# Kernel tuning notes

Hardware: AMD Instinct MI355X
Metric: run time of the kernel (lower is better)

The kernel has to match this reference:

```python
import jax, jax.numpy as jnp
import numpy as np
import math

N = 400000          # nodes at finest depth
E = 2000000         # edges = N * avg_degree
B = 8               # batch of octrees
C_IN = 4            # input feature channels (channel_in)
N_EDGE_TYPE = 5
N_NODE_TYPE = 7     # depth - 1
AVG_DEGREE = 5
C_OUT = 32          # channels[depth_out]
TEMB_CH = 512       # channels[depth_stop]


def swish(v):
    return v * jax.nn.sigmoid(v)


def setup_inputs() -> dict:
    key = jax.random.key(0)
    ks = jax.random.split(key, 12)
    x = jax.random.normal(ks[0], (N, C_IN), jnp.float32)
    t = jax.random.uniform(ks[1], (B,), jnp.float32) * 1000.0
    edge_index = jax.random.randint(ks[2], (2, E), 0, N)
    edge_type = jax.random.randint(ks[3], (E,), 0, N_EDGE_TYPE)
    node_type = jax.random.randint(ks[4], (N,), 0, N_NODE_TYPE)
    batch_id = jax.random.randint(ks[5], (N,), 0, B)
    fan = N_EDGE_TYPE * (C_IN + N_NODE_TYPE)  # 55
    W_conv = jax.random.normal(ks[6], (fan, C_OUT), jnp.float32) / np.sqrt(fan)
    W1 = jax.random.normal(ks[7], (TEMB_CH // 4, TEMB_CH), jnp.float32) / np.sqrt(TEMB_CH // 4)
    b1 = jnp.zeros((TEMB_CH,), jnp.float32)
    W2 = jax.random.normal(ks[8], (TEMB_CH, TEMB_CH), jnp.float32) / np.sqrt(TEMB_CH)
    b2 = jnp.zeros((TEMB_CH,), jnp.float32)
    W_temb = jax.random.normal(ks[9], (TEMB_CH, C_OUT), jnp.float32) / np.sqrt(TEMB_CH)
    return dict(x=x, t=t, edge_index=edge_index, edge_type=edge_type,
                node_type=node_type, batch_id=batch_id, W_conv=W_conv,
                W1=W1, b1=b1, W2=W2, b2=b2, W_temb=W_temb)


def time_embedding(t, W1, b1, W2, b2):
    # TimeEmbedding.forward: sinusoidal embedding -> lin1 -> swish -> lin2
    half = TEMB_CH // 8  # n_channels // 8
    freqs = jnp.exp(jnp.arange(half, dtype=jnp.float32) * (-math.log(10000.0) / (half - 1)))
    ang = t[:, None] * freqs[None, :]             # [B, half]
    emb = jnp.concatenate([jnp.sin(ang), jnp.cos(ang)], axis=1)  # [B, 2*half]
    emb = swish(emb @ W1 + b1)
    return emb @ W2 + b2                           # [B, TEMB_CH]


def graph_conv(x, edge_index, edge_type, node_type, W_conv):
    # dual-octree GraphConv: one-hot node type, per-(node, edge_type) gather-scatter, dense mix
    oh = jax.nn.one_hot(node_type, N_NODE_TYPE, dtype=x.dtype)
    xh = jnp.concatenate([x, oh], axis=1)          # [N, C_IN + N_NODE_TYPE]
    row, col = edge_index[0], edge_index[1]
    idx = row * N_EDGE_TYPE + edge_type            # bucket per (dst node, edge type)
    agg = jax.ops.segment_sum(xh[col], idx, num_segments=N * N_EDGE_TYPE)
    agg = agg.reshape(N, N_EDGE_TYPE * xh.shape[1])
    return (agg @ W_conv) / AVG_DEGREE             # [N, C_OUT]


def reference(x, t, edge_index, edge_type, node_type, batch_id, W_conv, W1, b1, W2, b2, W_temb):
    h = graph_conv(x, edge_index, edge_type, node_type, W_conv)   # conv1 on input features
    temb = time_embedding(t, W1, b1, W2, b2)                       # [B, TEMB_CH]
    inj = swish(temb) @ W_temb                                     # project temb to node channels
    return h + inj[batch_id]                                       # per-node temb injection
```

## Files before the change

kernel.cpp:

```cpp
#include <hip/hip_runtime.h>
#include <hip/hip_fp16.h>


#define CH      4096
#define CW      2048
#define CWSH    11
#define WSZ     128
#define WSH     7
#define NBCMAX  512
#define CAP     2048

__device__ __forceinline__ unsigned pack2(float a, float b) {
    __half2 h = __floats2half2_rn(a, b);
    union { __half2 h; unsigned u; } cv; cv.h = h; return cv.u;
}
__device__ __forceinline__ float2 unpack2(unsigned u) {
    union { unsigned u; __half2 h; } cv; cv.u = u;
    return __half22float2(cv.h);
}

__global__ __launch_bounds__(256) void histW_kernel(
    const int* __restrict__ ei, int* __restrict__ counts,
    const float* __restrict__ x, uint2* __restrict__ xh,
    const float* __restrict__ t, const float* __restrict__ W1,
    float* __restrict__ h1acc, float* __restrict__ h2acc,
    float* __restrict__ inj,
    int E, int N, int NBC, int NCHP)
{
    int tid = threadIdx.x;
    if ((int)blockIdx.x >= NCHP) {
        int b = blockIdx.x - NCHP;
        __shared__ float emb[128];
        if (tid < 128) {
            const float kStep = 9.210340371976184f / 63.0f;
            int k = tid & 63;
            float ang = t[b] * expf(-(float)k * kStep);
            emb[tid] = (tid < 64) ? sinf(ang) : cosf(ang);
        }
        __syncthreads();
        for (int j = tid; j < 512; j += 256) {
            float a = 0.f;
            for (int k = 0; k < 128; ++k) a += emb[k] * W1[k * 512 + j];
            h1acc[b * 512 + j] = a;
            h2acc[b * 512 + j] = 0.f;
        }
        if (tid < 32) inj[b * 32 + tid] = 0.f;
        return;
    }
    __shared__ int h[NBCMAX];
    int c = blockIdx.x;
    for (int i = tid; i < NBC; i += 256) h[i] = 0;
    __syncthreads();
    int s = c * CH, e = min(s + CH, E);
    int nfull = (e - s) & ~3;
    for (int i0 = s + tid * 4; i0 < s + nfull; i0 += 1024) {
        int4 r4 = *(const int4*)&ei[i0];
        atomicAdd(&h[r4.x >> CWSH], 1);
        atomicAdd(&h[r4.y >> CWSH], 1);
        atomicAdd(&h[r4.z >> CWSH], 1);
        atomicAdd(&h[r4.w >> CWSH], 1);
    }
    for (int i = s + nfull + tid; i < e; i += 256)
        atomicAdd(&h[ei[i] >> CWSH], 1);
    __syncthreads();
    int* row = counts + (size_t)c * NBC;
    for (int b = tid; b < NBC; b += 256) row[b] = h[b];
    int per = (N + NCHP - 1) / NCHP;
    int n0 = c * per, n1 = min(n0 + per, N);
    for (int n = n0 + tid; n < n1; n += 256) {
        float4 v = ((const float4*)x)[n];
        uint2 p;
        p.x = pack2(v.x, v.y);
        p.y = pack2(v.z, v.w);
        xh[n] = p;
    }
}

__global__ __launch_bounds__(256) void scanA_kernel(
    const int* __restrict__ counts, int* __restrict__ bsums,
    const float* __restrict__ h1acc, const float* __restrict__ b1,
    const float* __restrict__ W2, float* __restrict__ h2acc,
    int M, int NBC, int LOGC, int nblkA)
{
    int tid = threadIdx.x;
    if ((int)blockIdx.x >= nblkA) {
        int p = blockIdx.x - nblkA;
        __shared__ float h1s[64];
        if (tid < 64) {
            int bb = tid >> 3, kk = tid & 7;
            int k = p * 8 + kk;
            float v = h1acc[bb * 512 + k] + b1[k];
            h1s[tid] = v / (1.f + expf(-v));
        }
        __syncthreads();
        for (int jj = 0; jj < 2; ++jj) {
            int j = tid + jj * 256;
            float acc[8] = {};
#pragma unroll
            for (int kk = 0; kk < 8; ++kk) {
                float w = W2[(p * 8 + kk) * 512 + j];
#pragma unroll
                for (int bb = 0; bb < 8; ++bb) acc[bb] += h1s[bb * 8 + kk] * w;
            }
#pragma unroll
            for (int bb = 0; bb < 8; ++bb)
                atomicAdd(&h2acc[bb * 512 + j], acc[bb]);
        }
        return;
    }
    __shared__ int s[256];
    int j0 = blockIdx.x * 4096 + tid * 16;
    int maskC = (1 << LOGC) - 1;
    int p = 0;
#pragma unroll
    for (int k = 0; k < 16; ++k) {
        int j = j0 + k;
        if (j < M) {
            int b = j >> LOGC, c = j & maskC;
            p += counts[(size_t)c * NBC + b];
        }
    }
    s[tid] = p; __syncthreads();
    for (int off = 128; off > 0; off >>= 1) {
        if (tid < off) s[tid] += s[tid + off];
        __syncthreads();
    }
    if (tid == 0) bsums[blockIdx.x] = s[0];
}

__global__ __launch_bounds__(1024) void scanB_kernel(
    int* __restrict__ bsums, int* __restrict__ bstart, int nblk, int NBC, int E)
{
    __shared__ int s[1024];
    int tid = threadIdx.x;
    int v = (tid < nblk) ? bsums[tid] : 0;
    s[tid] = v; __syncthreads();
    for (int off = 1; off < 1024; off <<= 1) {
        int u = (tid >= off) ? s[tid - off] : 0;
        __syncthreads();
        s[tid] += u;
        __syncthreads();
    }
    if (tid < nblk) bsums[tid] = s[tid] - v;
    if (tid == 0) bstart[NBC] = E;
}

__global__ __launch_bounds__(256) void scanC_kernel(
    const int* __restrict__ counts, const int* __restrict__ bsums,
    int* __restrict__ base, int* __restrict__ bstart,
    const float* __restrict__ h2acc, const float* __restrict__ b2,
    const float* __restrict__ Wt, float* __restrict__ inj,
    int M, int NBC, int LOGC, int nblkA)
{
    int tid = threadIdx.x;
    if ((int)blockIdx.x >= nblkA) {
        int ks = blockIdx.x - nblkA;
        __shared__ float sws[8][64];
        for (int i = tid; i < 512; i += 256) {
            int b = i >> 6, kk = i & 63;
            int k = ks * 64 + kk;
            float v = h2acc[b * 512 + k] + b2[k];
            sws[b][kk] = v / (1.f + expf(-v));
        }
        __syncthreads();
        int b = tid >> 5, c = tid & 31;
        float acc = 0.f;
        for (int kk = 0; kk < 64; ++kk)
            acc += sws[b][kk] * Wt[(ks * 64 + kk) * 32 + c];
        atomicAdd(&inj[tid], acc);
        return;
    }
    __shared__ int s[256];
    int j0 = blockIdx.x * 4096 + tid * 16;
    int maskC = (1 << LOGC) - 1;
    int v[16]; int p = 0;
#pragma unroll
    for (int k = 0; k < 16; ++k) {
        int j = j0 + k;
        v[k] = 0;
        if (j < M) {
            int b = j >> LOGC, c = j & maskC;
            v[k] = counts[(size_t)c * NBC + b];
        }
        p += v[k];
    }
    s[tid] = p; __syncthreads();
    for (int off = 1; off < 256; off <<= 1) {
        int u = (tid >= off) ? s[tid - off] : 0;
        __syncthreads();
        s[tid] += u;
        __syncthreads();
    }
    int run = bsums[blockIdx.x] + (s[tid] - p);
#pragma unroll
    for (int k = 0; k < 16; ++k) {
        int j = j0 + k;
        if (j < M) {
            base[j] = run;
            if ((j & maskC) == 0) bstart[j >> LOGC] = run;
            run += v[k];
        }
    }
}

__global__ __launch_bounds__(512) void scatter_kernel(
    const int* __restrict__ ei, const int* __restrict__ etype,
    const int* __restrict__ ntype, const int* __restrict__ base,
    uint2* __restrict__ rec, int E, int NBC, int LOGC)
{
    __shared__ int cur[NBCMAX];
    int tid = threadIdx.x;
    int nwg = gridDim.x;
    int q = nwg >> 3, r = nwg & 7;
    int xcd = blockIdx.x & 7, idx = blockIdx.x >> 3;
    int c = (xcd < r) ? xcd * (q + 1) + idx
                      : r * (q + 1) + (xcd - r) * q + idx;
    for (int b = tid; b < NBC; b += 512)
        cur[b] = base[((size_t)b << LOGC) + c];
    __syncthreads();
    int s = c * CH, e = min(s + CH, E);
    int nfull = (e - s) & ~3;
    for (int i0 = s + tid * 4; i0 < s + nfull; i0 += 2048) {
        int4 r4 = *(const int4*)&ei[i0];
        int4 c4 = *(const int4*)&ei[E + i0];
        int4 t4 = *(const int4*)&etype[i0];
#pragma unroll
        for (int k = 0; k < 4; ++k) {
            int row = (&r4.x)[k], col = (&c4.x)[k], T = (&t4.x)[k];
            int nt = ntype[col];
            int b = row >> CWSH;
            int slot = atomicAdd(&cur[b], 1);
            uint2 rc;
            rc.x = (unsigned)col | ((unsigned)T << 19) | ((unsigned)nt << 22);
            rc.y = (unsigned)(row & (CW - 1));
            rec[slot] = rc;
        }
    }
    for (int i = s + nfull + tid; i < e; i += 512) {
        int row = ei[i], col = ei[E + i];
        int T = etype[i], nt = ntype[col];
        int b = row >> CWSH;
        int slot = atomicAdd(&cur[b], 1);
        uint2 rc;
        rc.x = (unsigned)col | ((unsigned)T << 19) | ((unsigned)nt << 22);
        rc.y = (unsigned)(row & (CW - 1));
        rec[slot] = rc;
    }
}

__global__ __launch_bounds__(1024) void repack_kernel(
    const int* __restrict__ bstart, const uint2* __restrict__ rec,
    unsigned* __restrict__ rec2, int* __restrict__ nodeStart,
    int NBC, int N, int E)
{
    __shared__ int hist[CW];
    __shared__ int sc[1024];
    int tid = threadIdx.x;
    int b = blockIdx.x;
    for (int i = tid; i < CW; i += 1024) hist[i] = 0;
    __syncthreads();
    int s = bstart[b], e = bstart[b + 1];
    for (int i = s + tid; i < e; i += 1024)
        atomicAdd(&hist[rec[i].y], 1);
    __syncthreads();
    int a0 = hist[2 * tid], a1 = hist[2 * tid + 1];
    int tsum = a0 + a1;
    sc[tid] = tsum; __syncthreads();
    for (int off = 1; off < 1024; off <<= 1) {
        int u = (tid >= off) ? sc[tid - off] : 0;
        __syncthreads();
        sc[tid] += u;
        __syncthreads();
    }
    int excl = sc[tid] - tsum;
    hist[2 * tid]     = s + excl;
    hist[2 * tid + 1] = s + excl + a0;
    __syncthreads();
    int nbase = b * CW;
    for (int l = tid; l < CW; l += 1024) {
        int n = nbase + l;
        if (n < N) nodeStart[n] = hist[l];
    }
    if (b == NBC - 1 && tid == 0) nodeStart[N] = E;
    __syncthreads();
    for (int i = s + tid; i < e; i += 1024) {
        uint2 rc = rec[i];
        int slot = atomicAdd(&hist[rc.y], 1);
        rec2[slot] = rc.x;
    }
}

__global__ __launch_bounds__(512) void consume_kernel(
    const int* __restrict__ nodeStart, const unsigned* __restrict__ rec2,
    const uint2* __restrict__ xh, const float* __restrict__ Wc,
    const int* __restrict__ batch, const float* __restrict__ inj,
    float* __restrict__ out, int N)
{
    __shared__ int seg[WSZ + 1];
    __shared__ unsigned smeta[CAP];
    __shared__ unsigned sx01[CAP];
    __shared__ unsigned sx23[CAP];
    int tid = threadIdx.x;
    int f = blockIdx.x;
    int node0 = f << WSH;
    int nodes = N - node0; if (nodes > WSZ) nodes = WSZ;

    for (int i = tid; i <= nodes; i += 512) seg[i] = nodeStart[node0 + i];
    __syncthreads();
    int s = seg[0], e = seg[nodes];

    int nl = tid & (WSZ - 1);
    int myS = (nl < nodes) ? seg[nl] : e;
    int myE = (nl < nodes) ? seg[nl + 1] : e;

    float acc[20] = {};
    int cnt0[5] = {}, cnt1[5] = {};
    for (int base = s; base < e; base += CAP) {
        int w = e - base; if (w > CAP) w = CAP;
        __syncthreads();
        for (int i = tid; i < w; i += 512) {
            unsigned u = rec2[base + i];
            smeta[i] = u;
            uint2 p = xh[u & 0x7FFFFu];
            sx01[i] = p.x;
            sx23[i] = p.y;
        }
        __syncthreads();
        int lo = myS > base ? myS : base;
        int hi = myE < base + w ? myE : base + w;
        for (int j = lo; j < hi; ++j) {
            int k = j - base;
            unsigned u = smeta[k];
            int T  = (int)((u >> 19) & 7u);
            int nt = (int)((u >> 22) & 7u);
            float2 x01 = unpack2(sx01[k]);
            float2 x23 = unpack2(sx23[k]);
            int lob = (nt < 4) ? (1 << (nt * 8)) : 0;
            int hib = (nt >= 4) ? (1 << ((nt - 4) * 8)) : 0;
#pragma unroll
            for (int tt = 0; tt < 5; ++tt) {
                bool m = (T == tt);
                acc[tt * 4 + 0] += m ? x01.x : 0.f;
                acc[tt * 4 + 1] += m ? x01.y : 0.f;
                acc[tt * 4 + 2] += m ? x23.x : 0.f;
                acc[tt * 4 + 3] += m ? x23.y : 0.f;
                cnt0[tt] += m ? lob : 0;
                cnt1[tt] += m ? hib : 0;
            }
        }
    }

    if (nl < nodes) {
        int hf = __builtin_amdgcn_readfirstlane((int)tid >> 7);
        const float4* wq = (const float4*)Wc;
        float4 o0 = {0.f, 0.f, 0.f, 0.f}, o1 = o0;
#pragma unroll
        for (int f2 = 0; f2 < 55; ++f2) {
            const int tt = f2 / 11, j = f2 % 11;
            float a;
            if (j < 4) a = acc[tt * 4 + j];
            else {
                const int kk = j - 4;
                a = (kk < 4) ? (float)((cnt0[tt] >> (kk * 8)) & 255)
                             : (float)((cnt1[tt] >> ((kk - 4) * 8)) & 255);
            }
            float4 w0 = wq[f2 * 8 + hf * 2];
            float4 w1 = wq[f2 * 8 + hf * 2 + 1];
            o0.x += a * w0.x; o0.y += a * w0.y; o0.z += a * w0.z; o0.w += a * w0.w;
            o1.x += a * w1.x; o1.y += a * w1.y; o1.z += a * w1.z; o1.w += a * w1.w;
        }
        int n = node0 + nl;
        int bb = batch[n];
        const float4* iv = ((const float4*)inj) + bb * 8 + hf * 2;
        float4 i0 = iv[0], i1 = iv[1];
        float4 r0, r1;
        r0.x = i0.x + 0.2f * o0.x; r0.y = i0.y + 0.2f * o0.y;
        r0.z = i0.z + 0.2f * o0.z; r0.w = i0.w + 0.2f * o0.w;
        r1.x = i1.x + 0.2f * o1.x; r1.y = i1.y + 0.2f * o1.y;
        r1.z = i1.z + 0.2f * o1.z; r1.w = i1.w + 0.2f * o1.w;
        float4* op = ((float4*)out) + (size_t)n * 8 + hf * 2;
        op[0] = r0; op[1] = r1;
    }
}

__global__ __launch_bounds__(256) void temb_fused_kernel(
    const float* __restrict__ t,
    const float* __restrict__ W1, const float* __restrict__ b1,
    const float* __restrict__ W2, const float* __restrict__ b2,
    const float* __restrict__ Wt, float* __restrict__ inj)
{
    int b = blockIdx.x;
    int tid = threadIdx.x;
    __shared__ float emb[128];
    __shared__ float s1[512];
    __shared__ float s2[512];
    __shared__ float red[256];
    float tv = t[b];
    if (tid < 128) {
        const float kStep = 9.210340371976184f / 63.0f;
        int k = tid & 63;
        float ang = tv * expf(-(float)k * kStep);
        emb[tid] = (tid < 64) ? sinf(ang) : cosf(ang);
    }
    __syncthreads();
    {
        float a0 = 0.f, a1 = 0.f;
        for (int k = 0; k < 128; ++k) {
            float e = emb[k];
            a0 += e * W1[k * 512 + tid];
            a1 += e * W1[k * 512 + tid + 256];
        }
        float v0 = a0 + b1[tid], v1 = a1 + b1[tid + 256];
        s1[tid]       = v0 / (1.0f + expf(-v0));
        s1[tid + 256] = v1 / (1.0f + expf(-v1));
    }
    __syncthreads();
    {
        float a0 = 0.f, a1 = 0.f;
        for (int k = 0; k < 512; ++k) {
            float e = s1[k];
            a0 += e * W2[k * 512 + tid];
            a1 += e * W2[k * 512 + tid + 256];
        }
        float v0 = a0 + b2[tid], v1 = a1 + b2[tid + 256];
        s2[tid]       = v0 / (1.0f + expf(-v0));
        s2[tid + 256] = v1 / (1.0f + expf(-v1));
    }
    __syncthreads();
    {
        int c = tid & 31, seg = tid >> 5;
        float acc = 0.f;
        int k0 = seg * 64;
        for (int k = k0; k < k0 + 64; ++k)
            acc += s2[k] * Wt[k * 32 + c];
        red[tid] = acc;
        __syncthreads();
        if (tid < 32) {
            float s = 0.f;
#pragma unroll
            for (int g = 0; g < 8; ++g) s += red[g * 32 + tid];
            inj[b * 32 + tid] = s;
        }
    }
}

__global__ __launch_bounds__(256) void init_kernel(
    const int* __restrict__ batch_id, const float* __restrict__ inj,
    float4* __restrict__ out, int N)
{
    int gid = blockIdx.x * 256 + threadIdx.x;
    if (gid >= N * 8) return;
    int n = gid >> 3, q = gid & 7;
    int b = batch_id[n];
    out[gid] = ((const float4*)inj)[b * 8 + q];
}

__global__ __launch_bounds__(256) void edge_direct_kernel(
    const int* __restrict__ ei, const int* __restrict__ etype,
    const int* __restrict__ ntype, const float* __restrict__ x,
    const float* __restrict__ Wc, float* __restrict__ out, int E)
{
    __shared__ float Ws[55 * 32];
    for (int i = threadIdx.x; i < 55 * 32; i += 256) Ws[i] = Wc[i];
    __syncthreads();
    unsigned total = (unsigned)E * 32u;
    unsigned stride = gridDim.x * 256u;
    for (unsigned idx = blockIdx.x * 256u + threadIdx.x; idx < total;
         idx += stride) {
        int e = (int)(idx >> 5);
        int c = (int)(idx & 31);
        int row = ei[e];
        int col = ei[E + e];
        int T = etype[e];
        int nt = ntype[col];
        float4 xv = ((const float4*)x)[col];
        const float* wb = Ws + T * 352;
        float y = xv.x * wb[c] + xv.y * wb[32 + c] + xv.z * wb[64 + c] +
                  xv.w * wb[96 + c] + wb[(4 + nt) * 32 + c];
        atomicAdd(out + (size_t)row * 32 + c, y * 0.2f);
    }
}

extern "C" void kernel_launch(void* const* d_in, const int* in_sizes, int n_in,
                              void* d_out, int out_size, void* d_ws, size_t ws_size,
                              hipStream_t stream) {
    const float* x     = (const float*)d_in[0];
    const float* t     = (const float*)d_in[1];
    const int*   ei    = (const int*)d_in[2];
    const int*   etype = (const int*)d_in[3];
    const int*   ntype = (const int*)d_in[4];
    const int*   batch = (const int*)d_in[5];
    const float* Wc    = (const float*)d_in[6];
    const float* W1    = (const float*)d_in[7];
    const float* b1    = (const float*)d_in[8];
    const float* W2    = (const float*)d_in[9];
    const float* b2    = (const float*)d_in[10];
    const float* Wt    = (const float*)d_in[11];
    float* out = (float*)d_out;

    int E = in_sizes[3];
    int N = in_sizes[4];

    int NBC = (N + CW - 1) >> CWSH;
    int NFr = (N + WSZ - 1) >> WSH;
    int NCH = (E + CH - 1) / CH;
    int NCHP = 1, LOGC = 0;
    while (NCHP < NCH) { NCHP <<= 1; ++LOGC; }
    size_t M = (size_t)NBC << LOGC;
    int nblkA = (int)((M + 4095) / 4096);

    float* ws     = (float*)d_ws;
    float* h1acc  = ws;
    float* h2acc  = ws + 4096;
    float* inj    = ws + 8192;
    uint2* xh     = (uint2*)(ws + 8448);
    int*   counts = (int*)(ws + 8448 + 2 * (size_t)N);
    int*   base   = counts + M;
    int*   bsums  = base + M;
    int*   bstart = bsums + 1024;
    int*   nodeSt = bstart + NBC + 1;
    size_t recOff = 8448 + 2 * (size_t)N + 2 * M + 1024 + (NBC + 1) +
                    ((size_t)N + 1);
    recOff = (recOff + 1) & ~(size_t)1;
    uint2*    rec  = (uint2*)(ws + recOff);
    unsigned* rec2 = (unsigned*)(ws + recOff + 2 * (size_t)E);

    size_t needBytes = (recOff + 3 * (size_t)E) * 4;
    bool okay = (NBC <= NBCMAX) && (nblkA <= 1024) && (ws_size >= needBytes) &&
                (N <= NBCMAX * CW) && ((E & 3) == 0) && (M < (size_t)1 << 30);

    if (okay) {
        histW_kernel<<<NCHP + 8, 256, 0, stream>>>(
            ei, counts, x, xh, t, W1, h1acc, h2acc, inj, E, N, NBC, NCHP);
        scanA_kernel<<<nblkA + 64, 256, 0, stream>>>(
            counts, bsums, h1acc, b1, W2, h2acc, (int)M, NBC, LOGC, nblkA);
        scanB_kernel<<<1, 1024, 0, stream>>>(bsums, bstart, nblkA, NBC, E);
        scanC_kernel<<<nblkA + 8, 256, 0, stream>>>(
            counts, bsums, base, bstart, h2acc, b2, Wt, inj,
            (int)M, NBC, LOGC, nblkA);
        scatter_kernel<<<NCH, 512, 0, stream>>>(
            ei, etype, ntype, base, rec, E, NBC, LOGC);
        repack_kernel<<<NBC, 1024, 0, stream>>>(
            bstart, rec, rec2, nodeSt, NBC, N, E);
        consume_kernel<<<NFr, 512, 0, stream>>>(
            nodeSt, rec2, xh, Wc, batch, inj, out, N);
    } else {
        temb_fused_kernel<<<8, 256, 0, stream>>>(t, W1, b1, W2, b2, Wt, inj);
        init_kernel<<<(N * 8 + 255) / 256, 256, 0, stream>>>(
            batch, inj, (float4*)out, N);
        edge_direct_kernel<<<16384, 256, 0, stream>>>(
            ei, etype, ntype, x, Wc, out, E);
    }
}
```

Baseline: 222.1 us.

## Precompute per-node degree histograms, drop repack counting pass, split consume edges across threads

```diff
diff --git a/kernel.cpp b/kernel.cpp
--- a/kernel.cpp
+++ b/kernel.cpp
@@ -2,7 +2,7 @@
 #include <hip/hip_fp16.h>
 
 
-#define CH      4096
+#define CH      2048
 #define CW      2048
 #define CWSH    11
 #define WSZ     128
@@ -21,6 +21,7 @@
 
 __global__ __launch_bounds__(256) void histW_kernel(
     const int* __restrict__ ei, int* __restrict__ counts,
+    int* __restrict__ nodeRep,
     const float* __restrict__ x, uint2* __restrict__ xh,
     const float* __restrict__ t, const float* __restrict__ W1,
     float* __restrict__ h1acc, float* __restrict__ h2acc,
@@ -51,6 +52,7 @@
     int c = blockIdx.x;
     for (int i = tid; i < NBC; i += 256) h[i] = 0;
     __syncthreads();
+    int* rep = nodeRep + (size_t)(blockIdx.x & 7) * N;
     int s = c * CH, e = min(s + CH, E);
     int nfull = (e - s) & ~3;
     for (int i0 = s + tid * 4; i0 < s + nfull; i0 += 1024) {
@@ -59,12 +61,19 @@
         atomicAdd(&h[r4.y >> CWSH], 1);
         atomicAdd(&h[r4.z >> CWSH], 1);
         atomicAdd(&h[r4.w >> CWSH], 1);
-    }
-    for (int i = s + nfull + tid; i < e; i += 256)
-        atomicAdd(&h[ei[i] >> CWSH], 1);
-    __syncthreads();
-    int* row = counts + (size_t)c * NBC;
-    for (int b = tid; b < NBC; b += 256) row[b] = h[b];
+        atomicAdd(&rep[r4.x], 1);
+        atomicAdd(&rep[r4.y], 1);
+        atomicAdd(&rep[r4.z], 1);
+        atomicAdd(&rep[r4.w], 1);
+    }
+    for (int i = s + nfull + tid; i < e; i += 256) {
+        int row = ei[i];
+        atomicAdd(&h[row >> CWSH], 1);
+        atomicAdd(&rep[row], 1);
+    }
+    __syncthreads();
+    int* rowp = counts + (size_t)c * NBC;
+    for (int b = tid; b < NBC; b += 256) rowp[b] = h[b];
     int per = (N + NCHP - 1) / NCHP;
     int n0 = c * per, n1 = min(n0 + per, N);
     for (int n = n0 + tid; n < n1; n += 256) {
@@ -249,22 +258,25 @@
 }
 
 __global__ __launch_bounds__(1024) void repack_kernel(
-    const int* __restrict__ bstart, const uint2* __restrict__ rec,
-    unsigned* __restrict__ rec2, int* __restrict__ nodeStart,
-    int NBC, int N, int E)
+    const int* __restrict__ bstart, const int* __restrict__ nodeRep,
+    const uint2* __restrict__ rec, unsigned* __restrict__ rec2,
+    int* __restrict__ nodeStart, int NBC, int N, int E)
 {
     __shared__ int hist[CW];
     __shared__ int sc[1024];
     int tid = threadIdx.x;
     int b = blockIdx.x;
-    for (int i = tid; i < CW; i += 1024) hist[i] = 0;
-    __syncthreads();
+    int nbase = b * CW;
     int s = bstart[b], e = bstart[b + 1];
-    for (int i = s + tid; i < e; i += 1024)
-        atomicAdd(&hist[rec[i].y], 1);
-    __syncthreads();
-    int a0 = hist[2 * tid], a1 = hist[2 * tid + 1];
-    int tsum = a0 + a1;
+    int n0 = nbase + 2 * tid, n1 = n0 + 1;
+    int c0 = 0, c1 = 0;
+#pragma unroll
+    for (int r = 0; r < 8; ++r) {
+        const int* rp = nodeRep + (size_t)r * N;
+        if (n0 < N) c0 += rp[n0];
+        if (n1 < N) c1 += rp[n1];
+    }
+    int tsum = c0 + c1;
     sc[tid] = tsum; __syncthreads();
     for (int off = 1; off < 1024; off <<= 1) {
         int u = (tid >= off) ? sc[tid - off] : 0;
@@ -274,9 +286,8 @@
     }
     int excl = sc[tid] - tsum;
     hist[2 * tid]     = s + excl;
-    hist[2 * tid + 1] = s + excl + a0;
-    __syncthreads();
-    int nbase = b * CW;
+    hist[2 * tid + 1] = s + excl + c0;
+    __syncthreads();
     for (int l = tid; l < CW; l += 1024) {
         int n = nbase + l;
         if (n < N) nodeStart[n] = hist[l];
@@ -297,9 +308,10 @@
     float* __restrict__ out, int N)
 {
     __shared__ int seg[WSZ + 1];
-    __shared__ unsigned smeta[CAP];
-    __shared__ unsigned sx01[CAP];
-    __shared__ unsigned sx23[CAP];
+    __shared__ unsigned sbuf[3 * CAP];
+    unsigned* smeta = sbuf;
+    unsigned* sx01  = sbuf + CAP;
+    unsigned* sx23  = sbuf + 2 * CAP;
     int tid = threadIdx.x;
     int f = blockIdx.x;
     int node0 = f << WSH;
@@ -310,6 +322,7 @@
     int s = seg[0], e = seg[nodes];
 
     int nl = tid & (WSZ - 1);
+    int rep = tid >> 7;
     int myS = (nl < nodes) ? seg[nl] : e;
     int myE = (nl < nodes) ? seg[nl + 1] : e;
 
@@ -326,9 +339,11 @@
             sx23[i] = p.y;
         }
         __syncthreads();
-        int lo = myS > base ? myS : base;
-        int hi = myE < base + w ? myE : base + w;
-        for (int j = lo; j < hi; ++j) {
+        int jstart = myS + rep;
+        if (jstart < base)
+            jstart += ((base - jstart + 3) >> 2) << 2;
+        int jend = myE < base + w ? myE : base + w;
+        for (int j = jstart; j < jend; j += 4) {
             int k = j - base;
             unsigned u = smeta[k];
             int T  = (int)((u >> 19) & 7u);
@@ -350,8 +365,44 @@
         }
     }
 
+    {
+        float* redf = (float*)sbuf;
+        int*   redi = (int*)sbuf;
+        int wslot = nl * 43 + rep * 10;
+        int rbase = nl * 43;
+#pragma unroll
+        for (int p = 0; p < 3; ++p) {
+            __syncthreads();
+            if (p < 2) {
+#pragma unroll
+                for (int i = 0; i < 10; ++i) redf[wslot + i] = acc[p * 10 + i];
+            } else {
+#pragma unroll
+                for (int i = 0; i < 5; ++i) {
+                    redi[wslot + i]     = cnt0[i];
+                    redi[wslot + 5 + i] = cnt1[i];
+                }
+            }
+            __syncthreads();
+            if (p < 2) {
+#pragma unroll
+                for (int i = 0; i < 10; ++i)
+                    acc[p * 10 + i] = redf[rbase + i] + redf[rbase + 10 + i] +
+                                      redf[rbase + 20 + i] + redf[rbase + 30 + i];
+            } else {
+#pragma unroll
+                for (int i = 0; i < 5; ++i) {
+                    cnt0[i] = redi[rbase + i] + redi[rbase + 10 + i] +
+                              redi[rbase + 20 + i] + redi[rbase + 30 + i];
+                    cnt1[i] = redi[rbase + 5 + i] + redi[rbase + 15 + i] +
+                              redi[rbase + 25 + i] + redi[rbase + 35 + i];
+                }
+            }
+        }
+    }
+
     if (nl < nodes) {
-        int hf = __builtin_amdgcn_readfirstlane((int)tid >> 7);
+        int hf = __builtin_amdgcn_readfirstlane(rep);
         const float4* wq = (const float4*)Wc;
         float4 o0 = {0.f, 0.f, 0.f, 0.f}, o1 = o0;
 #pragma unroll
@@ -514,13 +565,14 @@
     float* h2acc  = ws + 4096;
     float* inj    = ws + 8192;
     uint2* xh     = (uint2*)(ws + 8448);
-    int*   counts = (int*)(ws + 8448 + 2 * (size_t)N);
+    int*   nodeRep = (int*)(ws + 8448 + 2 * (size_t)N);
+    int*   counts = nodeRep + 8 * (size_t)N;
     int*   base   = counts + M;
     int*   bsums  = base + M;
     int*   bstart = bsums + 1024;
     int*   nodeSt = bstart + NBC + 1;
-    size_t recOff = 8448 + 2 * (size_t)N + 2 * M + 1024 + (NBC + 1) +
-                    ((size_t)N + 1);
+    size_t recOff = 8448 + 2 * (size_t)N + 8 * (size_t)N + 2 * M + 1024 +
+                    (NBC + 1) + ((size_t)N + 1);
     recOff = (recOff + 1) & ~(size_t)1;
     uint2*    rec  = (uint2*)(ws + recOff);
     unsigned* rec2 = (unsigned*)(ws + recOff + 2 * (size_t)E);
@@ -530,8 +582,11 @@
                 (N <= NBCMAX * CW) && ((E & 3) == 0) && (M < (size_t)1 << 30);
 
     if (okay) {
+        hipMemsetAsync(nodeRep, 0, 8 * (size_t)N * 4, stream);
+
         histW_kernel<<<NCHP + 8, 256, 0, stream>>>(
-            ei, counts, x, xh, t, W1, h1acc, h2acc, inj, E, N, NBC, NCHP);
+            ei, counts, nodeRep, x, xh, t, W1, h1acc, h2acc, inj,
+            E, N, NBC, NCHP);
         scanA_kernel<<<nblkA + 64, 256, 0, stream>>>(
             counts, bsums, h1acc, b1, W2, h2acc, (int)M, NBC, LOGC, nblkA);
         scanB_kernel<<<1, 1024, 0, stream>>>(bsums, bstart, nblkA, NBC, E);
@@ -541,7 +596,7 @@
         scatter_kernel<<<NCH, 512, 0, stream>>>(
             ei, etype, ntype, base, rec, E, NBC, LOGC);
         repack_kernel<<<NBC, 1024, 0, stream>>>(
-            bstart, rec, rec2, nodeSt, NBC, N, E);
+            bstart, nodeRep, rec, rec2, nodeSt, NBC, N, E);
         consume_kernel<<<NFr, 512, 0, stream>>>(
             nodeSt, rec2, xh, Wc, batch, inj, out, N);
     } else {
```

After: 295.8 us. +33.2%, slower.

## Split per-node edge accumulation across four thread replicas with LDS reduction

Applied to the files above, without the earlier changes.

```diff
diff --git a/kernel.cpp b/kernel.cpp
--- a/kernel.cpp
+++ b/kernel.cpp
@@ -297,9 +297,10 @@
     float* __restrict__ out, int N)
 {
     __shared__ int seg[WSZ + 1];
-    __shared__ unsigned smeta[CAP];
-    __shared__ unsigned sx01[CAP];
-    __shared__ unsigned sx23[CAP];
+    __shared__ unsigned sbuf[3 * CAP];
+    unsigned* smeta = sbuf;
+    unsigned* sx01  = sbuf + CAP;
+    unsigned* sx23  = sbuf + 2 * CAP;
     int tid = threadIdx.x;
     int f = blockIdx.x;
     int node0 = f << WSH;
@@ -310,6 +311,7 @@
     int s = seg[0], e = seg[nodes];
 
     int nl = tid & (WSZ - 1);
+    int rep = tid >> 7;
     int myS = (nl < nodes) ? seg[nl] : e;
     int myE = (nl < nodes) ? seg[nl + 1] : e;
 
@@ -326,9 +328,11 @@
             sx23[i] = p.y;
         }
         __syncthreads();
-        int lo = myS > base ? myS : base;
-        int hi = myE < base + w ? myE : base + w;
-        for (int j = lo; j < hi; ++j) {
+        int jstart = myS + rep;
+        if (jstart < base)
+            jstart += ((base - jstart + 3) >> 2) << 2;
+        int jend = myE < base + w ? myE : base + w;
+        for (int j = jstart; j < jend; j += 4) {
             int k = j - base;
             unsigned u = smeta[k];
             int T  = (int)((u >> 19) & 7u);
@@ -350,8 +354,44 @@
         }
     }
 
+    {
+        float* redf = (float*)sbuf;
+        int*   redi = (int*)sbuf;
+        int wslot = nl * 43 + rep * 10;
+        int rbase = nl * 43;
+#pragma unroll
+        for (int p = 0; p < 3; ++p) {
+            __syncthreads();
+            if (p < 2) {
+#pragma unroll
+                for (int i = 0; i < 10; ++i) redf[wslot + i] = acc[p * 10 + i];
+            } else {
+#pragma unroll
+                for (int i = 0; i < 5; ++i) {
+                    redi[wslot + i]     = cnt0[i];
+                    redi[wslot + 5 + i] = cnt1[i];
+                }
+            }
+            __syncthreads();
+            if (p < 2) {
+#pragma unroll
+                for (int i = 0; i < 10; ++i)
+                    acc[p * 10 + i] = redf[rbase + i] + redf[rbase + 10 + i] +
+                                      redf[rbase + 20 + i] + redf[rbase + 30 + i];
+            } else {
+#pragma unroll
+                for (int i = 0; i < 5; ++i) {
+                    cnt0[i] = redi[rbase + i] + redi[rbase + 10 + i] +
+                              redi[rbase + 20 + i] + redi[rbase + 30 + i];
+                    cnt1[i] = redi[rbase + 5 + i] + redi[rbase + 15 + i] +
+                              redi[rbase + 25 + i] + redi[rbase + 35 + i];
+                }
+            }
+        }
+    }
+
     if (nl < nodes) {
-        int hf = __builtin_amdgcn_readfirstlane((int)tid >> 7);
+        int hf = __builtin_amdgcn_readfirstlane(rep);
         const float4* wq = (const float4*)Wc;
         float4 o0 = {0.f, 0.f, 0.f, 0.f}, o1 = o0;
 #pragma unroll
```

Measured after the change: 225.5 us. Within noise of the previous version (+1.5%).
